# Kernel optimization log

Hardware: AMD Instinct MI355X
Metric: run time of the kernel (lower is better)

Reference implementation:

```python
import jax, jax.numpy as jnp
import numpy as np

B, S, T = 512, 512, 128


def setup_inputs() -> dict:
    key = jax.random.key(0)
    k1, k2, k3, k4, k5 = jax.random.split(key, 5)
    emissions = jax.random.normal(k1, (B, S, T), dtype=jnp.float32)
    tags = jax.random.randint(k2, (B, S), 0, T, dtype=jnp.int32)
    mask = jnp.ones((B, S), dtype=jnp.int32)
    start_transitions = jax.random.uniform(k3, (T,), minval=-0.1, maxval=0.1, dtype=jnp.float32)
    end_transitions = jax.random.uniform(k4, (T,), minval=-0.1, maxval=0.1, dtype=jnp.float32)
    transitions = jax.random.uniform(k5, (T, T), minval=-0.1, maxval=0.1, dtype=jnp.float32)
    return {"emissions": emissions, "tags": tags, "mask": mask,
            "start_transitions": start_transitions,
            "end_transitions": end_transitions,
            "transitions": transitions}


def reference(emissions, tags, mask, start_transitions, end_transitions, transitions):
    b, s, t = emissions.shape
    maskf = mask.astype(emissions.dtype)
    barange = jnp.arange(b)

    # ---- numerator: score of the gold path (vectorized over timesteps) ----
    score = start_transitions[tags[:, 0]] + emissions[barange, 0, tags[:, 0]]
    # transition scores tags[i-1] -> tags[i], shape (B, S-1)
    trans_steps = transitions[tags[:, :-1], tags[:, 1:]]
    # emission score of gold tag at each step, shape (B, S)
    em_steps = jnp.take_along_axis(emissions, tags[:, :, None], axis=2)[:, :, 0]
    score = score + jnp.sum((trans_steps + em_steps[:, 1:]) * maskf[:, 1:], axis=1)
    seq_ends = mask.astype(jnp.int32).sum(axis=1) - 1
    last_tags = tags[barange, seq_ends]
    score = score + end_transitions[last_tags]

    # ---- denominator: log partition via forward recurrence (lax.scan) ----
    init = start_transitions[None, :] + emissions[:, 0, :]  # (B, T)

    def step(scores, inp):
        em_i, m_i = inp  # (B, T), (B,)
        # (B, T_prev, T_next) semiring matmul in log-space
        nxt = jax.nn.logsumexp(
            scores[:, :, None] + transitions[None, :, :] + em_i[:, None, :], axis=1)
        scores = jnp.where(m_i[:, None] > 0, nxt, scores)
        return scores, None

    ems = jnp.moveaxis(emissions[:, 1:, :], 1, 0)  # (S-1, B, T)
    ms = jnp.moveaxis(mask[:, 1:], 1, 0)           # (S-1, B)
    final, _ = jax.lax.scan(step, init, (ems, ms))
    denom = jax.nn.logsumexp(final + end_transitions[None, :], axis=1)  # (B,)

    return jnp.sum(score - denom)
```

## Files before the change

kernel.cpp:

```cpp
#include <hip/hip_runtime.h>
#include <math.h>


#define T 128
#define SLEN 512
#define BATCH 512

typedef float v2f __attribute__((ext_vector_type(2)));

__global__ __launch_bounds__(256, 2) void fwd_kernel(
    const float* __restrict__ em, const int* __restrict__ tags,
    const int* __restrict__ mask, const float* __restrict__ startT,
    const float* __restrict__ endT, const float* __restrict__ trans,
    float* __restrict__ ws)
{
    const int tid = threadIdx.x;
    const int rg  = tid & 7;
    const int cg  = tid >> 3;
    const int q   = rg & 3;
    const int b   = blockIdx.x;
    const int jc  = 4 * cg + q;
    const float* emb = em + (size_t)b * SLEN * T;
    const int*   mk  = mask + (size_t)b * SLEN;

    int craw[4], slot[4];
#pragma unroll
    for (int i = 0; i < 4; ++i) {
        craw[i] = 4 * rg + ((i + rg) & 3);
        slot[i] = craw[i] ^ ((craw[i] & 16) ? 4 : 0);
    }

    v2f Elo[4][4], Ehi[4][4];
#pragma unroll
    for (int i = 0; i < 4; ++i) {
        const int r0 = 4 * craw[i];
#pragma unroll
        for (int qq = 0; qq < 4; ++qq) {
            const int col = 4 * cg + qq;
            Elo[i][qq] = (v2f){ __expf(trans[(r0 + 0) * T + col]),
                                __expf(trans[(r0 + 1) * T + col]) };
            Ehi[i][qq] = (v2f){ __expf(trans[(r0 + 2) * T + col]),
                                __expf(trans[(r0 + 3) * T + col]) };
        }
    }

    __shared__ __align__(16) float4 psh[2][32];
    __shared__ float sig_sh[2];
    __shared__ float redm[4], reds[4], redn[4];
    __shared__ int   redc[4];

    const char* rp[4];
#pragma unroll
    for (int i = 0; i < 4; ++i)
        rp[i] = (const char*)&psh[0][0] + slot[i] * 16;
    const int scg = cg ^ ((cg & 16) ? 4 : 0);
    char* wp = (char*)&psh[0][0] + scg * 16 + q * 4;

    float score = startT[jc] + emb[jc];
    if (rg < 4) *(float*)(wp + 512) = __expf(score);
    if (tid == 0) sig_sh[1] = score;
    float sigma = 0.f;

    float emv[4], emn[4];
    int   mkv[4], mkn[4];
#pragma unroll
    for (int k = 0; k < 4; ++k) { emv[k] = (emb + (1 + k) * T)[jc]; mkv[k] = mk[1 + k]; }
    __syncthreads();

    const bool lb0 = (rg & 1) != 0, lb1 = (rg & 2) != 0;

    for (int s0 = 1; s0 < SLEN; s0 += 4) {
#pragma unroll
        for (int k = 0; k < 4; ++k) {
            int ss = s0 + 4 + k; ss = (ss < SLEN) ? ss : (SLEN - 1);
            emn[k] = (emb + ss * T)[jc];
            mkn[k] = mk[ss];
        }
#pragma unroll
        for (int k = 0; k < 4; ++k) {
            const int s = s0 + k;
            if (s < SLEN) {
                const int cur = (1 + k) & 1;
                v2f a0 = {0.f, 0.f}, a1 = a0, a2 = a0, a3 = a0;
#pragma unroll
                for (int i = 0; i < 4; ++i) {
                    const float4 pv = *(const float4*)(rp[i] + cur * 512);
                    const v2f plo = {pv.x, pv.y}, phi = {pv.z, pv.w};
                    a0 = __builtin_elementwise_fma(plo, Elo[i][0], a0);
                    a0 = __builtin_elementwise_fma(phi, Ehi[i][0], a0);
                    a1 = __builtin_elementwise_fma(plo, Elo[i][1], a1);
                    a1 = __builtin_elementwise_fma(phi, Ehi[i][1], a1);
                    a2 = __builtin_elementwise_fma(plo, Elo[i][2], a2);
                    a2 = __builtin_elementwise_fma(phi, Ehi[i][2], a2);
                    a3 = __builtin_elementwise_fma(plo, Elo[i][3], a3);
                    a3 = __builtin_elementwise_fma(phi, Ehi[i][3], a3);
                }
                const float c0 = a0.x + a0.y, c1 = a1.x + a1.y;
                const float c2 = a2.x + a2.y, c3 = a3.x + a3.y;
                float P  = (lb0 ? c1 : c0) + __shfl_xor(lb0 ? c0 : c1, 1);
                float P2 = (lb0 ? c3 : c2) + __shfl_xor(lb0 ? c2 : c3, 1);
                float t  = (lb1 ? P2 : P) + __shfl_xor(lb1 ? P : P2, 2);
                t += __shfl_xor(t, 4);
                const float sig_next = sig_sh[cur];
                const float n = sigma + __logf(t) + emv[k];
                score = (mkv[k] > 0) ? n : score;
                const float pp = __expf(score - sig_next);
                if (rg < 4) *(float*)(wp + (cur ^ 1) * 512) = pp;
                if (tid == 0) sig_sh[cur ^ 1] = score;
                sigma = sig_next;
                __syncthreads();
            }
        }
#pragma unroll
        for (int k = 0; k < 4; ++k) { emv[k] = emn[k]; mkv[k] = mkn[k]; }
    }

    const int wid = tid >> 6;
    float v = score + endT[jc];
    float m = v;
#pragma unroll
    for (int off = 32; off; off >>= 1) m = fmaxf(m, __shfl_xor(m, off));
    if ((tid & 63) == 0) redm[wid] = m;
    __syncthreads();
    float M = redm[0];
#pragma unroll
    for (int i = 1; i < 4; ++i) M = fmaxf(M, redm[i]);
    float sm = __expf(v - M) * 0.5f;
#pragma unroll
    for (int off = 32; off; off >>= 1) sm += __shfl_xor(sm, off);
    if ((tid & 63) == 0) reds[wid] = sm;

    const int* tg = tags + (size_t)b * SLEN;
    float nv = 0.f; int cnt = 0;
#pragma unroll
    for (int rep = 0; rep < 2; ++rep) {
        const int s = tid + 256 * rep;
        const int mm = mk[s];
        cnt += (mm != 0);
        if (s >= 1 && mm > 0)
            nv += trans[tg[s - 1] * T + tg[s]] + emb[s * T + tg[s]];
    }
#pragma unroll
    for (int off = 32; off; off >>= 1) {
        nv  += __shfl_xor(nv, off);
        cnt += __shfl_xor(cnt, off);
    }
    if ((tid & 63) == 0) { redn[wid] = nv; redc[wid] = cnt; }
    __syncthreads();
    if (tid == 0) {
        float ssum = 0.f, nsum = 0.f; int seqlen = 0;
#pragma unroll
        for (int i = 0; i < 4; ++i) {
            ssum += reds[i]; nsum += redn[i]; seqlen += redc[i];
        }
        const float denom = M + __logf(ssum);
        const int t0 = tg[0], tl = tg[seqlen - 1];
        ws[b] = (startT[t0] + emb[t0] + endT[tl] + nsum) - denom;
    }
}

__global__ __launch_bounds__(256) void reduce_kernel(
    const float* __restrict__ ws, float* __restrict__ out)
{
    const int t = threadIdx.x;
    float local = 0.f;
    for (int i = t; i < BATCH; i += 256) local += ws[i];
    __shared__ float rf[256];
    rf[t] = local;
    __syncthreads();
    for (int off = 128; off > 0; off >>= 1) {
        if (t < off) rf[t] += rf[t + off];
        __syncthreads();
    }
    if (t == 0) out[0] = rf[0];
}

extern "C" void kernel_launch(void* const* d_in, const int* in_sizes, int n_in,
                              void* d_out, int out_size, void* d_ws, size_t ws_size,
                              hipStream_t stream)
{
    const float* emissions = (const float*)d_in[0];
    const int*   tags      = (const int*)d_in[1];
    const int*   mask      = (const int*)d_in[2];
    const float* startT    = (const float*)d_in[3];
    const float* endT      = (const float*)d_in[4];
    const float* trans     = (const float*)d_in[5];
    float* out = (float*)d_out;
    float* ws  = (float*)d_ws;

    fwd_kernel<<<BATCH, 256, 0, stream>>>(emissions, tags, mask, startT, endT, trans, ws);
    reduce_kernel<<<1, 256, 0, stream>>>(ws, out);
}
```

Baseline: 398.0 us.

## Run CRF forward recurrence in scaled linear space with reference-element normalization

Reformulates the forward recurrence so the probabilities stay in linear space. Each step is normalized by the previous step's first element, read from shared memory, and the log of that scale is accumulated in a double. This removes the per-step log and exp on the critical path, the thread-0 sigma store to shared memory, and the max-reduction at the end. Emissions are exponentiated when prefetched. The risk is numerical: normalizing by one element rather than the max could underflow or overflow for other inputs, and the double accumulation adds FP64 work on every step.

```diff
diff --git a/kernel.cpp b/kernel.cpp
--- a/kernel.cpp
+++ b/kernel.cpp
@@ -45,8 +45,7 @@
     }
 
     __shared__ __align__(16) float4 psh[2][32];
-    __shared__ float sig_sh[2];
-    __shared__ float redm[4], reds[4], redn[4];
+    __shared__ float reds[4], redn[4];
     __shared__ int   redc[4];
 
     const char* rp[4];
@@ -55,16 +54,19 @@
         rp[i] = (const char*)&psh[0][0] + slot[i] * 16;
     const int scg = cg ^ ((cg & 16) ? 4 : 0);
     char* wp = (char*)&psh[0][0] + scg * 16 + q * 4;
+    const char* srefp = (const char*)&psh[0][0];
 
-    float score = startT[jc] + emb[jc];
-    if (rg < 4) *(float*)(wp + 512) = __expf(score);
-    if (tid == 0) sig_sh[1] = score;
-    float sigma = 0.f;
+    float pprev = __expf(startT[jc] + emb[jc]);
+    if (rg < 4) *(float*)(wp + 512) = pprev;
+    double Ld = 0.0;
 
     float emv[4], emn[4];
     int   mkv[4], mkn[4];
 #pragma unroll
-    for (int k = 0; k < 4; ++k) { emv[k] = (emb + (1 + k) * T)[jc]; mkv[k] = mk[1 + k]; }
+    for (int k = 0; k < 4; ++k) {
+        emv[k] = __expf((emb + (1 + k) * T)[jc]);
+        mkv[k] = mk[1 + k];
+    }
     __syncthreads();
 
     const bool lb0 = (rg & 1) != 0, lb1 = (rg & 2) != 0;
@@ -81,6 +83,12 @@
             const int s = s0 + k;
             if (s < SLEN) {
                 const int cur = (1 + k) & 1;
+                const float sref0 = *(const float*)(srefp + cur * 512);
+                const float srefc = fmaxf(sref0, 1e-30f);
+                const float cc = __builtin_amdgcn_rcpf(srefc);
+                const float f  = emv[k] * cc;
+                Ld += (double)__logf(srefc);
+
                 v2f a0 = {0.f, 0.f}, a1 = a0, a2 = a0, a3 = a0;
 #pragma unroll
                 for (int i = 0; i < 4; ++i) {
@@ -101,31 +109,19 @@
                 float P2 = (lb0 ? c3 : c2) + __shfl_xor(lb0 ? c2 : c3, 1);
                 float t  = (lb1 ? P2 : P) + __shfl_xor(lb1 ? P : P2, 2);
                 t += __shfl_xor(t, 4);
-                const float sig_next = sig_sh[cur];
-                const float n = sigma + __logf(t) + emv[k];
-                score = (mkv[k] > 0) ? n : score;
-                const float pp = __expf(score - sig_next);
-                if (rg < 4) *(float*)(wp + (cur ^ 1) * 512) = pp;
-                if (tid == 0) sig_sh[cur ^ 1] = score;
-                sigma = sig_next;
+                const float pn = t * f;
+                const float pm = pprev * cc;
+                pprev = (mkv[k] > 0) ? pn : pm;
+                if (rg < 4) *(float*)(wp + (cur ^ 1) * 512) = pprev;
                 __syncthreads();
             }
         }
 #pragma unroll
-        for (int k = 0; k < 4; ++k) { emv[k] = emn[k]; mkv[k] = mkn[k]; }
+        for (int k = 0; k < 4; ++k) { emv[k] = __expf(emn[k]); mkv[k] = mkn[k]; }
     }
 
     const int wid = tid >> 6;
-    float v = score + endT[jc];
-    float m = v;
-#pragma unroll
-    for (int off = 32; off; off >>= 1) m = fmaxf(m, __shfl_xor(m, off));
-    if ((tid & 63) == 0) redm[wid] = m;
-    __syncthreads();
-    float M = redm[0];
-#pragma unroll
-    for (int i = 1; i < 4; ++i) M = fmaxf(M, redm[i]);
-    float sm = __expf(v - M) * 0.5f;
+    float sm = (rg < 4) ? pprev * __expf(endT[jc]) : 0.f;
 #pragma unroll
     for (int off = 32; off; off >>= 1) sm += __shfl_xor(sm, off);
     if ((tid & 63) == 0) reds[wid] = sm;
@@ -153,7 +149,7 @@
         for (int i = 0; i < 4; ++i) {
             ssum += reds[i]; nsum += redn[i]; seqlen += redc[i];
         }
-        const float denom = M + __logf(ssum);
+        const float denom = __logf(ssum) + (float)Ld;
         const int t0 = tg[0], tl = tg[seqlen - 1];
         ws[b] = (startT[t0] + emb[t0] + endT[tl] + nsum) - denom;
     }
```

After: 383.5 us. -3.7%, faster.
